# Kernel tuning notes

Hardware: AMD Instinct MI355X
Metric: run time of the kernel (lower is better)

## Reference

```python
import jax, jax.numpy as jnp
import numpy as np

B, C, D, H, W = 8, 256, 128, 64, 64  # batch, in_channels, inter_dim, spatial
BN_EPS = 1e-5


def setup_inputs() -> dict:
    key = jax.random.key(0)
    ks = jax.random.split(key, 6)
    s_c = 1.0 / np.sqrt(C)
    s_d = 1.0 / np.sqrt(D)
    return {
        "x": jax.random.normal(ks[0], (B, C, H, W), dtype=jnp.float32),
        # 1x1 conv kernels, stored as [out_ch, in_ch]
        "theta_w": jax.random.normal(ks[1], (D, C), dtype=jnp.float32) * s_c,
        "phi_w": jax.random.normal(ks[2], (D, C), dtype=jnp.float32) * s_c,
        "g_w": jax.random.normal(ks[3], (D, C), dtype=jnp.float32) * s_c,
        "w_w": jax.random.normal(ks[4], (C, D), dtype=jnp.float32) * s_d,
        "w_b": jnp.zeros((C,), dtype=jnp.float32),
        "bn_gamma": jnp.ones((C,), dtype=jnp.float32),
        "bn_beta": jnp.zeros((C,), dtype=jnp.float32),
    }


def reference(x, theta_w, phi_w, g_w, w_w, w_b, bn_gamma, bn_beta):
    Bs, Cs, Hs, Ws = x.shape
    N = Hs * Ws
    xf = x.reshape(Bs, Cs, N)  # flatten spatial -> [B, C, N]

    # 1x1 convs (bias=False) == per-position channel matmuls
    theta = jnp.einsum('dc,bcn->bnd', theta_w, xf)  # [B, N, D]
    phi = jnp.einsum('dc,bcn->bdn', phi_w, xf)      # [B, D, N]
    g = jnp.einsum('dc,bcn->bnd', g_w, xf)          # [B, N, D]

    # embedded-Gaussian attention: softmax(theta @ phi) @ g
    f = jnp.einsum('bnd,bdm->bnm', theta, phi)      # [B, N, N]
    f_div_C = jax.nn.softmax(f, axis=-1)
    y = jnp.einsum('bnm,bmd->bnd', f_div_C, g)      # [B, N, D]

    # output projection W (1x1 conv with bias)
    w_y = jnp.einsum('cd,bnd->bcn', w_w, y) + w_b[None, :, None]  # [B, C, N]

    # BatchNorm (training mode: batch statistics, biased variance)
    mean = w_y.mean(axis=(0, 2))
    var = jnp.mean(jnp.square(w_y - mean[None, :, None]), axis=(0, 2))
    scale = (bn_gamma * jax.lax.rsqrt(var + BN_EPS))[None, :, None]
    w_y = (w_y - mean[None, :, None]) * scale + bn_beta[None, :, None]

    z = w_y + xf  # residual
    return z.reshape(Bs, Cs, Hs, Ws)
```

## Files before the change

kernel.cpp:

```cpp
#include <hip/hip_runtime.h>

#define BB 8
#define CC 256
#define DD 128
#define NN 4096
#define BN_EPS 1e-5f

typedef _Float16 f16;
typedef _Float16 half8 __attribute__((ext_vector_type(8)));
typedef _Float16 half2t __attribute__((ext_vector_type(2)));
typedef float f32x4 __attribute__((ext_vector_type(4)));

__device__ __forceinline__ f32x4 mfma16(half8 a, half8 b, f32x4 c) {
  return __builtin_amdgcn_mfma_f32_16x16x32_f16(a, b, c, 0, 0, 0);
}

__device__ __forceinline__ void gload_lds16(const void* g, void* l) {
  __builtin_amdgcn_global_load_lds((const __attribute__((address_space(1))) void*)g,
                                   (__attribute__((address_space(3))) void*)l, 16, 0, 0);
}

__device__ __forceinline__ half2t pkrtz(float a, float b) {
  auto t = __builtin_amdgcn_cvt_pkrtz(a, b);
  return __builtin_bit_cast(half2t, t);
}

#define EXP2(x) __builtin_amdgcn_exp2f(x)

#define PERM32(i) ((((i) >> 2) & 3) * 8 + (((i) >> 4) & 1) * 4 + ((i) & 3))

__global__ void k_cast_weights(const float* __restrict__ tw, const float* __restrict__ pw,
                               const float* __restrict__ gw, const float* __restrict__ ww,
                               f16* __restrict__ Wcat, f16* __restrict__ Wwh,
                               float* __restrict__ stats) {
  int i = blockIdx.x * 256 + threadIdx.x;
  if (i < 32768) Wcat[i] = (f16)tw[i];
  else if (i < 65536) Wcat[i] = (f16)pw[i - 32768];
  else if (i < 98304) Wcat[i] = (f16)gw[i - 65536];
  else if (i < 131072) Wwh[i - 98304] = (f16)ww[i - 98304];
  if (i < 512) stats[i] = 0.f;
}

__global__ __launch_bounds__(256) void k_gemm1(const float* __restrict__ x, const f16* __restrict__ Wcat,
                                               f16* __restrict__ T, f16* __restrict__ P,
                                               f16* __restrict__ Gdn) {
  __shared__ char xls[32768];
  __shared__ char gls[16384];
  int b = blockIdx.y;
  int n0 = blockIdx.x * 64;
  int tid = threadIdx.x;
  int lane = tid & 63, wave = tid >> 6;
  int lr = lane & 15, lg = lane >> 4;
  int wr = wave >> 1, wc = wave & 1;

  {
    int c = tid;
    const float* src = x + ((size_t)b * CC + c) * NN + n0;
#pragma unroll
    for (int n4 = 0; n4 < 64; n4 += 4) {
      f32x4 v = *(const f32x4*)(src + n4);
#pragma unroll
      for (int k = 0; k < 4; ++k) {
        int n = n4 + k;
        *(f16*)(xls + n * 512 + ((((c >> 3) ^ (n & 7)) * 8 + (c & 7)) * 2)) = (f16)v[k];
      }
    }
  }
  __syncthreads();

  half8 a[2][8];
#pragma unroll
  for (int i = 0; i < 2; ++i) {
    int nloc = wr * 32 + i * 16 + lr;
#pragma unroll
    for (int k0 = 0; k0 < 8; ++k0)
      a[i][k0] = *(const half8*)(xls + nloc * 512 + (((k0 * 4 + lg) ^ (nloc & 7)) << 4));
  }

  size_t base = (size_t)b * NN + n0;
#pragma unroll
  for (int yb = 0; yb < 6; ++yb) {
    int c0 = yb * 64 + wc * 32;
    f32x4 acc[2][2] = {};
#pragma unroll
    for (int k0 = 0; k0 < 8; ++k0) {
      half8 w[2];
      for (int j = 0; j < 2; ++j)
        w[j] = *(const half8*)(Wcat + (size_t)(c0 + j * 16 + lr) * CC + k0 * 32 + lg * 8);
      for (int i = 0; i < 2; ++i)
        for (int j = 0; j < 2; ++j)
          acc[i][j] = mfma16(a[i][k0], w[j], acc[i][j]);
    }
    if (yb < 4) {
      f16* dst = (yb < 2) ? T : P;
      int cl0 = (yb & 1) * 64 + wc * 32;
      for (int i = 0; i < 2; ++i)
        for (int j = 0; j < 2; ++j)
          for (int r = 0; r < 4; ++r) {
            int row = wr * 32 + i * 16 + lg * 4 + r;
            int col = cl0 + j * 16 + lr;
            dst[(base + row) * DD + col] = (f16)acc[i][j][r];
          }
    } else {
      for (int i = 0; i < 2; ++i)
        for (int j = 0; j < 2; ++j)
          for (int r = 0; r < 4; ++r) {
            int n = wr * 32 + i * 16 + lg * 4 + r;
            int d = (yb - 4) * 64 + wc * 32 + j * 16 + lr;
            *(f16*)(gls + n * 256 + ((((d >> 3) ^ (n & 7)) * 8 + (d & 7)) * 2)) = (f16)acc[i][j][r];
          }
    }
  }
  __syncthreads();
  {
    int d = tid >> 1, nh = (tid & 1) * 32;
    f16 tmp[32];
#pragma unroll
    for (int k = 0; k < 32; ++k) {
      int n = nh + k;
      tmp[k] = *(const f16*)(gls + n * 256 + ((((d >> 3) ^ (n & 7)) * 8 + (d & 7)) * 2));
    }
    f16* dst = Gdn + ((size_t)b * DD + d) * NN + n0 + nh;
#pragma unroll
    for (int k = 0; k < 4; ++k)
      *(half8*)(dst + k * 8) = *(const half8*)(tmp + k * 8);
  }
}

__global__ __launch_bounds__(256, 4) void k_flash(const f16* __restrict__ T, const f16* __restrict__ P,
                                                  const f16* __restrict__ Gdn, f16* __restrict__ acc0,
                                                  f16* __restrict__ acc1, float* __restrict__ ml) {
  __shared__ char smem[32768];
  int bid = blockIdx.x;
  int b = bid & 7;
  int u = bid >> 3;
  int hf = u & 1;
  int qx = u >> 1;
  int tid = threadIdx.x;
  int lane = tid & 63, wave = tid >> 6;
  int lr = lane & 15, lg = lane >> 4;
  int q0 = qx * 64 + wave * 16;
  const f16* Tb = T + (size_t)b * NN * DD;
  const f16* Pb = P + ((size_t)b * NN + hf * 2048) * DD;
  const f16* Vb = Gdn + (size_t)b * DD * NN + hf * 2048;
  int srcq = 4 * lg;

  const f16* kbase[2];
  const f16* vbase[2];
  char* kdst[2];
  char* vdst[2];
#pragma unroll
  for (int inst = 0; inst < 2; ++inst) {
    int t = inst * 256 + tid;
    int row = t >> 4, sp = t & 15, sl = sp ^ (row & 7);
    kbase[inst] = Pb + (size_t)PERM32(row) * DD + sl * 8;
    kdst[inst] = smem + (inst * 256 + wave * 64) * 16;
    int dv = t >> 2, gv = t & 3, glv = gv ^ ((dv >> 1) & 3);
    vbase[inst] = Vb + (size_t)dv * NN + glv * 8;
    vdst[inst] = smem + 16384 + (inst * 256 + wave * 64) * 16;
  }

  half8 qf[4];
  for (int ks = 0; ks < 4; ++ks) {
    half8 v = *(const half8*)(Tb + (size_t)(q0 + lr) * DD + ks * 32 + lg * 8);
    for (int j = 0; j < 8; ++j) v[j] *= (f16)1.44269504f;
    qf[ks] = v;
  }
  half8 ones;
  for (int j = 0; j < 8; ++j) ones[j] = (f16)1.f;

  f32x4 acc[8] = {};
  f32x4 lsum = {};
  float m_run = -1e30f;

#pragma unroll
  for (int inst = 0; inst < 2; ++inst) gload_lds16(kbase[inst], kdst[inst]);
#pragma unroll
  for (int inst = 0; inst < 2; ++inst) gload_lds16(vbase[inst], vdst[inst]);

  for (int kb = 0; kb < 64; ++kb) {
    int keyn = (kb < 63) ? kb * 32 + 32 : 0;
    int cur = (kb & 1) * 8192, nxt = ((kb + 1) & 1) * 8192;
    char* Kc = smem + cur;
    char* Vc = smem + 16384 + cur;

    size_t ko = (size_t)keyn * DD;
#pragma unroll
    for (int inst = 0; inst < 2; ++inst) gload_lds16(kbase[inst] + ko, kdst[inst] + nxt);
    asm volatile("s_waitcnt vmcnt(4)" ::: "memory");
    __builtin_amdgcn_sched_barrier(0);
    __builtin_amdgcn_s_barrier();
    __builtin_amdgcn_sched_barrier(0);

    f32x4 s[2];
    __builtin_amdgcn_s_setprio(1);
    for (int kt = 0; kt < 2; ++kt) {
      f32x4 t = {};
      for (int ks = 0; ks < 4; ++ks) {
        half8 kf = *(const half8*)(Kc + (kt * 16 + lr) * 256 + (((ks * 4 + lg) ^ (lr & 7)) << 4));
        t = mfma16(kf, qf[ks], t);
      }
      s[kt] = t;
    }
    __builtin_amdgcn_s_setprio(0);

    float mx = fmaxf(fmaxf(s[0][0], s[0][1]), fmaxf(s[0][2], s[0][3]));
    mx = fmaxf(mx, fmaxf(fmaxf(s[1][0], s[1][1]), fmaxf(s[1][2], s[1][3])));
    mx = fmaxf(mx, __shfl_xor(mx, 16));
    mx = fmaxf(mx, __shfl_xor(mx, 32));
    bool grow = mx > m_run + 11.5f;
    if (__ballot(grow)) {
      float mn = fmaxf(m_run, mx);
      float corr = EXP2(m_run - mn);
      m_run = mn;
      float c0 = __shfl(corr, srcq + 0), c1 = __shfl(corr, srcq + 1);
      float c2 = __shfl(corr, srcq + 2), c3 = __shfl(corr, srcq + 3);
      lsum[0] *= c0; lsum[1] *= c1; lsum[2] *= c2; lsum[3] *= c3;
      for (int nb = 0; nb < 8; ++nb) {
        acc[nb][0] *= c0; acc[nb][1] *= c1; acc[nb][2] *= c2; acc[nb][3] *= c3;
      }
    }
    for (int kt = 0; kt < 2; ++kt)
      for (int r = 0; r < 4; ++r)
        s[kt][r] = EXP2(s[kt][r] - m_run);

    half8 af;
    {
      union { half8 h8; half2t h2[4]; } un;
      un.h2[0] = pkrtz(s[0][0], s[0][1]);
      un.h2[1] = pkrtz(s[0][2], s[0][3]);
      un.h2[2] = pkrtz(s[1][0], s[1][1]);
      un.h2[3] = pkrtz(s[1][2], s[1][3]);
      af = un.h8;
    }
    lsum = mfma16(af, ones, lsum);

#pragma unroll
    for (int inst = 0; inst < 2; ++inst) gload_lds16(vbase[inst] + keyn, vdst[inst] + nxt);
    asm volatile("s_waitcnt vmcnt(4)" ::: "memory");
    __builtin_amdgcn_sched_barrier(0);
    __builtin_amdgcn_s_barrier();
    __builtin_amdgcn_sched_barrier(0);

    __builtin_amdgcn_s_setprio(1);
    for (int nb = 0; nb < 8; ++nb) {
      int d = nb * 16 + lr;
      half8 vf = *(const half8*)(Vc + d * 64 + ((lg ^ ((d >> 1) & 3)) << 4));
      acc[nb] = mfma16(af, vf, acc[nb]);
    }
    __builtin_amdgcn_s_setprio(0);
  }
  asm volatile("s_waitcnt vmcnt(0)" ::: "memory");

  size_t gq0 = (size_t)b * NN + q0;
  f16* A = (hf ? acc1 : acc0) + gq0 * DD;
  for (int nb = 0; nb < 8; ++nb)
    for (int r = 0; r < 4; ++r)
      A[(size_t)(lg * 4 + r) * DD + nb * 16 + lr] = (f16)acc[nb][r];
  float* mArr = ml + hf * 32768;
  float* lArr = ml + 65536 + hf * 32768;
  if (lg == 0) mArr[gq0 + lr] = m_run;
  if (lr == 0)
    for (int r = 0; r < 4; ++r) lArr[gq0 + lg * 4 + r] = lsum[r];
}

__global__ void k_merge(const f16* __restrict__ a0, const f16* __restrict__ a1,
                        const float* __restrict__ ml, f16* __restrict__ Y) {
  int idx = blockIdx.x * 256 + threadIdx.x;
  int q = idx >> 4, dc = (idx & 15) * 8;
  float m1 = ml[q], m2 = ml[32768 + q];
  float l1 = ml[65536 + q], l2 = ml[98304 + q];
  float mm = fmaxf(m1, m2);
  float c1 = EXP2(m1 - mm), c2 = EXP2(m2 - mm);
  float inv = 1.f / (l1 * c1 + l2 * c2);
  c1 *= inv; c2 *= inv;
  half8 va = *(const half8*)(a0 + (size_t)q * DD + dc);
  half8 vb = *(const half8*)(a1 + (size_t)q * DD + dc);
  half8 o;
  for (int j = 0; j < 8; ++j) o[j] = (f16)((float)va[j] * c1 + (float)vb[j] * c2);
  *(half8*)(Y + (size_t)q * DD + dc) = o;
}

__global__ __launch_bounds__(256) void k_gemm2(const f16* __restrict__ Y, const f16* __restrict__ Wwh,
                                               const float* __restrict__ wb, f16* __restrict__ wy,
                                               float* __restrict__ stats) {
  __shared__ float part[2][8][64];
  int lane = threadIdx.x & 63, wave = threadIdx.x >> 6;
  int lr = lane & 15, lg = lane >> 4;
  int wr = wave >> 1, wc = wave & 1;
  int c0 = blockIdx.y * 64 + wc * 32;
  half8 w[4][2];
  for (int k0 = 0; k0 < 4; ++k0)
    for (int j = 0; j < 2; ++j)
      w[k0][j] = *(const half8*)(Wwh + (size_t)(c0 + j * 16 + lr) * DD + k0 * 32 + lg * 8);
  float bias[2];
  for (int j = 0; j < 2; ++j) bias[j] = wb[c0 + j * 16 + lr];
  float ps[2][2] = {};
  for (int mt = 0; mt < 8; ++mt) {
    int m0 = (blockIdx.x * 8 + mt) * 64 + wr * 32;
    f32x4 acc[2][2] = {};
    for (int k0 = 0; k0 < 4; ++k0) {
      half8 a[2];
      for (int i = 0; i < 2; ++i)
        a[i] = *(const half8*)(Y + (size_t)(m0 + i * 16 + lr) * DD + k0 * 32 + lg * 8);
      for (int i = 0; i < 2; ++i)
        for (int j = 0; j < 2; ++j)
          acc[i][j] = mfma16(a[i], w[k0][j], acc[i][j]);
    }
    for (int i = 0; i < 2; ++i)
      for (int j = 0; j < 2; ++j)
        for (int r = 0; r < 4; ++r) {
          int row = m0 + i * 16 + lg * 4 + r;
          int col = c0 + j * 16 + lr;
          float v = acc[i][j][r] + bias[j];
          wy[(size_t)row * CC + col] = (f16)v;
          ps[j][0] += v;
          ps[j][1] += v * v;
        }
  }
  for (int j = 0; j < 2; ++j) {
    int colL = wc * 32 + j * 16 + lr;
    part[0][wr * 4 + lg][colL] = ps[j][0];
    part[1][wr * 4 + lg][colL] = ps[j][1];
  }
  __syncthreads();
  if (threadIdx.x < 128) {
    int metric = threadIdx.x >> 6, col = threadIdx.x & 63;
    float s = 0.f;
    for (int wtr = 0; wtr < 8; ++wtr) s += part[metric][wtr][col];
    atomicAdd(&stats[metric * CC + blockIdx.y * 64 + col], s);
  }
}

__global__ void k_bn_apply(const f16* __restrict__ wy, const float* __restrict__ x,
                           const float* __restrict__ stats, const float* __restrict__ gamma,
                           const float* __restrict__ beta, float* __restrict__ out) {
  __shared__ f16 tile[32][33];
  int b = blockIdx.z, c0 = blockIdx.y * 32, n0 = blockIdx.x * 32;
  int tx = threadIdx.x, ty = threadIdx.y;
  for (int j = 0; j < 4; ++j) {
    int nn = ty + j * 8;
    tile[nn][tx] = wy[((size_t)b * NN + n0 + nn) * CC + c0 + tx];
  }
  __syncthreads();
  const float inv_cnt = 1.f / (float)(BB * NN);
  for (int j = 0; j < 4; ++j) {
    int cc = ty + j * 8;
    int c = c0 + cc;
    float mean = stats[c] * inv_cnt;
    float var = stats[CC + c] * inv_cnt - mean * mean;
    float scale = gamma[c] * rsqrtf(var + BN_EPS);
    size_t oi = ((size_t)b * CC + c) * NN + n0 + tx;
    out[oi] = ((float)tile[tx][cc] - mean) * scale + beta[c] + x[oi];
  }
}

extern "C" void kernel_launch(void* const* d_in, const int* in_sizes, int n_in,
                              void* d_out, int out_size, void* d_ws, size_t ws_size,
                              hipStream_t stream) {
  const float* x = (const float*)d_in[0];
  const float* tw = (const float*)d_in[1];
  const float* pw = (const float*)d_in[2];
  const float* gw = (const float*)d_in[3];
  const float* ww = (const float*)d_in[4];
  const float* wb = (const float*)d_in[5];
  const float* gamma = (const float*)d_in[6];
  const float* beta = (const float*)d_in[7];
  float* out = (float*)d_out;
  char* ws = (char*)d_ws;

  f16* Wcat = (f16*)(ws + 0);
  f16* Wwh = (f16*)(ws + 196608);
  float* stats = (float*)(ws + 262144);
  float* ml = (float*)(ws + 524288);
  const size_t BASE = 1 << 20;
  f16* T = (f16*)(ws + BASE);
  f16* P = (f16*)(ws + BASE + 8388608);
  f16* Gdn = (f16*)(ws + BASE + 16777216);
  f16* Yb = (f16*)(ws + BASE + 25165824);
  f16* acc1 = (f16*)(ws + BASE + 33554432);
  f16* wy = (f16*)(ws + BASE + 41943040);

  k_cast_weights<<<512, 256, 0, stream>>>(tw, pw, gw, ww, Wcat, Wwh, stats);
  k_gemm1<<<dim3(NN / 64, BB), 256, 0, stream>>>(x, Wcat, T, P, Gdn);
  k_flash<<<1024, 256, 0, stream>>>(T, P, Gdn, Yb, acc1, ml);
  k_merge<<<2048, 256, 0, stream>>>(Yb, acc1, ml, Yb);
  k_gemm2<<<dim3(BB * NN / 512, CC / 64), 256, 0, stream>>>(Yb, Wwh, wb, wy, stats);
  k_bn_apply<<<dim3(NN / 32, CC / 32, BB), dim3(32, 8), 0, stream>>>(wy, x, stats, gamma, beta, out);
}
```

Measured before the change: 175.9 us.

## Process two query tiles per wave and split keys four ways in flash

Each wave now handles 32 queries (two 16-row tiles) and reuses every K and V fragment loaded from LDS for both tiles. This halves LDS reads per MFMA. To keep the grid at 1024 blocks, the key range is split into four 1024-key segments instead of two, and the merge kernel combines four partial results. The cost is more accumulator registers and more partial-output traffic through the merge, and the wy buffer now aliases the T region to fit the workspace.

```diff
diff --git a/kernel.cpp b/kernel.cpp
--- a/kernel.cpp
+++ b/kernel.cpp
@@ -128,21 +128,21 @@
 }
 
 __global__ __launch_bounds__(256, 4) void k_flash(const f16* __restrict__ T, const f16* __restrict__ P,
-                                                  const f16* __restrict__ Gdn, f16* __restrict__ acc0,
-                                                  f16* __restrict__ acc1, float* __restrict__ ml) {
+                                                  const f16* __restrict__ Gdn, f16* __restrict__ accs,
+                                                  float* __restrict__ ml) {
   __shared__ char smem[32768];
   int bid = blockIdx.x;
   int b = bid & 7;
   int u = bid >> 3;
-  int hf = u & 1;
-  int qx = u >> 1;
+  int hf = u & 3;
+  int qx = u >> 2;
   int tid = threadIdx.x;
   int lane = tid & 63, wave = tid >> 6;
   int lr = lane & 15, lg = lane >> 4;
-  int q0 = qx * 64 + wave * 16;
+  int q0 = qx * 128 + wave * 32;
   const f16* Tb = T + (size_t)b * NN * DD;
-  const f16* Pb = P + ((size_t)b * NN + hf * 2048) * DD;
-  const f16* Vb = Gdn + (size_t)b * DD * NN + hf * 2048;
+  const f16* Pb = P + ((size_t)b * NN + hf * 1024) * DD;
+  const f16* Vb = Gdn + (size_t)b * DD * NN + hf * 1024;
   int srcq = 4 * lg;
 
   const f16* kbase[2];
@@ -160,26 +160,27 @@
     vdst[inst] = smem + 16384 + (inst * 256 + wave * 64) * 16;
   }
 
-  half8 qf[4];
-  for (int ks = 0; ks < 4; ++ks) {
-    half8 v = *(const half8*)(Tb + (size_t)(q0 + lr) * DD + ks * 32 + lg * 8);
-    for (int j = 0; j < 8; ++j) v[j] *= (f16)1.44269504f;
-    qf[ks] = v;
-  }
+  half8 qf[2][4];
+  for (int qt = 0; qt < 2; ++qt)
+    for (int ks = 0; ks < 4; ++ks) {
+      half8 v = *(const half8*)(Tb + (size_t)(q0 + qt * 16 + lr) * DD + ks * 32 + lg * 8);
+      for (int j = 0; j < 8; ++j) v[j] *= (f16)1.44269504f;
+      qf[qt][ks] = v;
+    }
   half8 ones;
   for (int j = 0; j < 8; ++j) ones[j] = (f16)1.f;
 
-  f32x4 acc[8] = {};
-  f32x4 lsum = {};
-  float m_run = -1e30f;
+  f32x4 acc[2][8] = {};
+  f32x4 lsum[2] = {};
+  float m_run[2] = {-1e30f, -1e30f};
 
 #pragma unroll
   for (int inst = 0; inst < 2; ++inst) gload_lds16(kbase[inst], kdst[inst]);
 #pragma unroll
   for (int inst = 0; inst < 2; ++inst) gload_lds16(vbase[inst], vdst[inst]);
 
-  for (int kb = 0; kb < 64; ++kb) {
-    int keyn = (kb < 63) ? kb * 32 + 32 : 0;
+  for (int kb = 0; kb < 32; ++kb) {
+    int keyn = (kb < 31) ? kb * 32 + 32 : 0;
     int cur = (kb & 1) * 8192, nxt = ((kb + 1) & 1) * 8192;
     char* Kc = smem + cur;
     char* Vc = smem + 16384 + cur;
@@ -192,48 +193,50 @@
     __builtin_amdgcn_s_barrier();
     __builtin_amdgcn_sched_barrier(0);
 
-    f32x4 s[2];
+    f32x4 s[2][2];
     __builtin_amdgcn_s_setprio(1);
     for (int kt = 0; kt < 2; ++kt) {
-      f32x4 t = {};
-      for (int ks = 0; ks < 4; ++ks) {
-        half8 kf = *(const half8*)(Kc + (kt * 16 + lr) * 256 + (((ks * 4 + lg) ^ (lr & 7)) << 4));
-        t = mfma16(kf, qf[ks], t);
+      half8 kf[4];
+      for (int ks = 0; ks < 4; ++ks)
+        kf[ks] = *(const half8*)(Kc + (kt * 16 + lr) * 256 + (((ks * 4 + lg) ^ (lr & 7)) << 4));
+      for (int qt = 0; qt < 2; ++qt) {
+        f32x4 t = {};
+        for (int ks = 0; ks < 4; ++ks) t = mfma16(kf[ks], qf[qt][ks], t);
+        s[qt][kt] = t;
       }
-      s[kt] = t;
     }
     __builtin_amdgcn_s_setprio(0);
 
-    float mx = fmaxf(fmaxf(s[0][0], s[0][1]), fmaxf(s[0][2], s[0][3]));
-    mx = fmaxf(mx, fmaxf(fmaxf(s[1][0], s[1][1]), fmaxf(s[1][2], s[1][3])));
-    mx = fmaxf(mx, __shfl_xor(mx, 16));
-    mx = fmaxf(mx, __shfl_xor(mx, 32));
-    bool grow = mx > m_run + 11.5f;
-    if (__ballot(grow)) {
-      float mn = fmaxf(m_run, mx);
-      float corr = EXP2(m_run - mn);
-      m_run = mn;
-      float c0 = __shfl(corr, srcq + 0), c1 = __shfl(corr, srcq + 1);
-      float c2 = __shfl(corr, srcq + 2), c3 = __shfl(corr, srcq + 3);
-      lsum[0] *= c0; lsum[1] *= c1; lsum[2] *= c2; lsum[3] *= c3;
-      for (int nb = 0; nb < 8; ++nb) {
-        acc[nb][0] *= c0; acc[nb][1] *= c1; acc[nb][2] *= c2; acc[nb][3] *= c3;
+    half8 af[2];
+    for (int qt = 0; qt < 2; ++qt) {
+      float mx = fmaxf(fmaxf(s[qt][0][0], s[qt][0][1]), fmaxf(s[qt][0][2], s[qt][0][3]));
+      mx = fmaxf(mx, fmaxf(fmaxf(s[qt][1][0], s[qt][1][1]), fmaxf(s[qt][1][2], s[qt][1][3])));
+      mx = fmaxf(mx, __shfl_xor(mx, 16));
+      mx = fmaxf(mx, __shfl_xor(mx, 32));
+      bool grow = mx > m_run[qt] + 11.5f;
+      if (__ballot(grow)) {
+        float mn = fmaxf(m_run[qt], mx);
+        float corr = EXP2(m_run[qt] - mn);
+        m_run[qt] = mn;
+        float c0 = __shfl(corr, srcq + 0), c1 = __shfl(corr, srcq + 1);
+        float c2 = __shfl(corr, srcq + 2), c3 = __shfl(corr, srcq + 3);
+        lsum[qt][0] *= c0; lsum[qt][1] *= c1; lsum[qt][2] *= c2; lsum[qt][3] *= c3;
+        for (int nb = 0; nb < 8; ++nb) {
+          acc[qt][nb][0] *= c0; acc[qt][nb][1] *= c1;
+          acc[qt][nb][2] *= c2; acc[qt][nb][3] *= c3;
+        }
       }
-    }
-    for (int kt = 0; kt < 2; ++kt)
-      for (int r = 0; r < 4; ++r)
-        s[kt][r] = EXP2(s[kt][r] - m_run);
-
-    half8 af;
-    {
+      for (int kt = 0; kt < 2; ++kt)
+        for (int r = 0; r < 4; ++r)
+          s[qt][kt][r] = EXP2(s[qt][kt][r] - m_run[qt]);
       union { half8 h8; half2t h2[4]; } un;
-      un.h2[0] = pkrtz(s[0][0], s[0][1]);
-      un.h2[1] = pkrtz(s[0][2], s[0][3]);
-      un.h2[2] = pkrtz(s[1][0], s[1][1]);
-      un.h2[3] = pkrtz(s[1][2], s[1][3]);
-      af = un.h8;
-    }
-    lsum = mfma16(af, ones, lsum);
+      un.h2[0] = pkrtz(s[qt][0][0], s[qt][0][1]);
+      un.h2[1] = pkrtz(s[qt][0][2], s[qt][0][3]);
+      un.h2[2] = pkrtz(s[qt][1][0], s[qt][1][1]);
+      un.h2[3] = pkrtz(s[qt][1][2], s[qt][1][3]);
+      af[qt] = un.h8;
+      lsum[qt] = mfma16(af[qt], ones, lsum[qt]);
+    }
 
 #pragma unroll
     for (int inst = 0; inst < 2; ++inst) gload_lds16(vbase[inst] + keyn, vdst[inst] + nxt);
@@ -246,39 +249,51 @@
     for (int nb = 0; nb < 8; ++nb) {
       int d = nb * 16 + lr;
       half8 vf = *(const half8*)(Vc + d * 64 + ((lg ^ ((d >> 1) & 3)) << 4));
-      acc[nb] = mfma16(af, vf, acc[nb]);
+      acc[0][nb] = mfma16(af[0], vf, acc[0][nb]);
+      acc[1][nb] = mfma16(af[1], vf, acc[1][nb]);
     }
     __builtin_amdgcn_s_setprio(0);
   }
   asm volatile("s_waitcnt vmcnt(0)" ::: "memory");
 
   size_t gq0 = (size_t)b * NN + q0;
-  f16* A = (hf ? acc1 : acc0) + gq0 * DD;
-  for (int nb = 0; nb < 8; ++nb)
-    for (int r = 0; r < 4; ++r)
-      A[(size_t)(lg * 4 + r) * DD + nb * 16 + lr] = (f16)acc[nb][r];
+  f16* A = accs + (size_t)hf * (BB * NN * DD) + gq0 * DD;
+  for (int qt = 0; qt < 2; ++qt)
+    for (int nb = 0; nb < 8; ++nb)
+      for (int r = 0; r < 4; ++r)
+        A[(size_t)(qt * 16 + lg * 4 + r) * DD + nb * 16 + lr] = (f16)acc[qt][nb][r];
   float* mArr = ml + hf * 32768;
-  float* lArr = ml + 65536 + hf * 32768;
-  if (lg == 0) mArr[gq0 + lr] = m_run;
+  float* lArr = ml + 131072 + hf * 32768;
+  if (lg == 0) {
+    mArr[gq0 + lr] = m_run[0];
+    mArr[gq0 + 16 + lr] = m_run[1];
+  }
   if (lr == 0)
-    for (int r = 0; r < 4; ++r) lArr[gq0 + lg * 4 + r] = lsum[r];
-}
-
-__global__ void k_merge(const f16* __restrict__ a0, const f16* __restrict__ a1,
-                        const float* __restrict__ ml, f16* __restrict__ Y) {
+    for (int r = 0; r < 4; ++r) {
+      lArr[gq0 + lg * 4 + r] = lsum[0][r];
+      lArr[gq0 + 16 + lg * 4 + r] = lsum[1][r];
+    }
+}
+
+__global__ void k_merge(f16* __restrict__ accs, const float* __restrict__ ml) {
   int idx = blockIdx.x * 256 + threadIdx.x;
   int q = idx >> 4, dc = (idx & 15) * 8;
-  float m1 = ml[q], m2 = ml[32768 + q];
-  float l1 = ml[65536 + q], l2 = ml[98304 + q];
-  float mm = fmaxf(m1, m2);
-  float c1 = EXP2(m1 - mm), c2 = EXP2(m2 - mm);
-  float inv = 1.f / (l1 * c1 + l2 * c2);
-  c1 *= inv; c2 *= inv;
-  half8 va = *(const half8*)(a0 + (size_t)q * DD + dc);
-  half8 vb = *(const half8*)(a1 + (size_t)q * DD + dc);
+  float m0 = ml[q], m1 = ml[32768 + q], m2 = ml[65536 + q], m3 = ml[98304 + q];
+  float l0 = ml[131072 + q], l1 = ml[163840 + q], l2 = ml[196608 + q], l3 = ml[229376 + q];
+  float mm = fmaxf(fmaxf(m0, m1), fmaxf(m2, m3));
+  float c0 = EXP2(m0 - mm), c1 = EXP2(m1 - mm), c2 = EXP2(m2 - mm), c3 = EXP2(m3 - mm);
+  float inv = 1.f / (l0 * c0 + l1 * c1 + l2 * c2 + l3 * c3);
+  c0 *= inv; c1 *= inv; c2 *= inv; c3 *= inv;
+  const size_t SEG = (size_t)BB * NN * DD;
+  size_t off = (size_t)q * DD + dc;
+  half8 v0 = *(const half8*)(accs + off);
+  half8 v1 = *(const half8*)(accs + SEG + off);
+  half8 v2 = *(const half8*)(accs + 2 * SEG + off);
+  half8 v3 = *(const half8*)(accs + 3 * SEG + off);
   half8 o;
-  for (int j = 0; j < 8; ++j) o[j] = (f16)((float)va[j] * c1 + (float)vb[j] * c2);
-  *(half8*)(Y + (size_t)q * DD + dc) = o;
+  for (int j = 0; j < 8; ++j)
+    o[j] = (f16)((float)v0[j] * c0 + (float)v1[j] * c1 + (float)v2[j] * c2 + (float)v3[j] * c3);
+  *(half8*)(accs + off) = o;
 }
 
 __global__ __launch_bounds__(256) void k_gemm2(const f16* __restrict__ Y, const f16* __restrict__ Wwh,
@@ -373,18 +388,17 @@
   f16* Wwh = (f16*)(ws + 196608);
   float* stats = (float*)(ws + 262144);
   float* ml = (float*)(ws + 524288);
-  const size_t BASE = 1 << 20;
+  const size_t BASE = 1 << 22;
   f16* T = (f16*)(ws + BASE);
   f16* P = (f16*)(ws + BASE + 8388608);
   f16* Gdn = (f16*)(ws + BASE + 16777216);
-  f16* Yb = (f16*)(ws + BASE + 25165824);
-  f16* acc1 = (f16*)(ws + BASE + 33554432);
-  f16* wy = (f16*)(ws + BASE + 41943040);
+  f16* accs = (f16*)(ws + BASE + 25165824);
+  f16* wy = (f16*)(ws + BASE);
 
   k_cast_weights<<<512, 256, 0, stream>>>(tw, pw, gw, ww, Wcat, Wwh, stats);
   k_gemm1<<<dim3(NN / 64, BB), 256, 0, stream>>>(x, Wcat, T, P, Gdn);
-  k_flash<<<1024, 256, 0, stream>>>(T, P, Gdn, Yb, acc1, ml);
-  k_merge<<<2048, 256, 0, stream>>>(Yb, acc1, ml, Yb);
-  k_gemm2<<<dim3(BB * NN / 512, CC / 64), 256, 0, stream>>>(Yb, Wwh, wb, wy, stats);
+  k_flash<<<1024, 256, 0, stream>>>(T, P, Gdn, accs, ml);
+  k_merge<<<2048, 256, 0, stream>>>(accs, ml);
+  k_gemm2<<<dim3(BB * NN / 512, CC / 64), 256, 0, stream>>>(accs, Wwh, wb, wy, stats);
   k_bn_apply<<<dim3(NN / 32, CC / 32, BB), dim3(32, 8), 0, stream>>>(wy, x, stats, gamma, beta, out);
 }
```

Measured after the change: 419.3 us. 138% more time.
